# Kernel optimization log

Hardware: AMD Instinct MI355X
Metric: run time of the kernel (lower is better)

Reference implementation:

```python
import jax, jax.numpy as jnp
import numpy as np
import math

ROPE_BASE = 10000.0
ALIBI_SLOPE = 2.0 ** (-8.0)  # _get_alibi_slopes(1) == [2**(-8*1/1)]


def _rope_cos_sin(T, d):
    inv_freq = 1.0 / (ROPE_BASE ** (jnp.arange(0, d, 2, dtype=jnp.float32) / d))
    t = jnp.arange(T, dtype=jnp.float32)
    freqs = jnp.einsum('i,j->ij', t, inv_freq)          # [T, d/2]
    emb = jnp.concatenate([freqs, freqs], axis=-1)      # [T, d]
    return jnp.cos(emb), jnp.sin(emb)


def _rotate_half(x):
    x1, x2 = jnp.split(x, 2, axis=-1)
    return jnp.concatenate([-x2, x1], axis=-1)


def setup_inputs() -> dict:
    key = jax.random.key(0)
    kq, kk, kv = jax.random.split(key, 3)
    B, T, H = 8, 2048, 256
    return {
        'q': jax.random.normal(kq, (B, T, H), dtype=jnp.float32),
        'k': jax.random.normal(kk, (B, T, H), dtype=jnp.float32),
        'v': jax.random.normal(kv, (B, T, H), dtype=jnp.float32),
    }


def reference(q, k, v):
    B, T, H = q.shape  # num_heads == 1, so head_dim == H
    cos, sin = _rope_cos_sin(T, H)                      # [T, H]
    qe = q * cos + _rotate_half(q) * sin                # [B, T, H]
    ke = k * cos + _rotate_half(k) * sin                # [B, T, H]

    scale = 1.0 / math.sqrt(H)
    scores = jnp.einsum('btd,bsd->bts', qe, ke) * scale  # [B, T, T]

    pos = jnp.arange(T)
    rel = (pos[None, :] - pos[:, None]).astype(jnp.float32)  # [T, T]
    alibi = (ALIBI_SLOPE * rel)[None, None, :, :]            # [1, 1, T, T]

    # torch broadcast: [B,T,T] + [1,1,T,T] -> [1,B,T,T]
    scores = scores + alibi
    attn = jax.nn.softmax(scores, axis=-1)              # [1, B, T, T]
    out = jnp.matmul(attn, v)                           # [1, B, T, H]
    return out
```

## Files before the change

kernel.cpp:

```cpp
#include <hip/hip_runtime.h>

#define B_ 8
#define T_ 2048
#define H_ 256
#define PSTR 40
#define SCALE2 0.0901684403f
#define SLOPE2 0.00563552752f
#define ELEMS ((size_t)B_ * T_ * H_)

typedef __attribute__((ext_vector_type(8))) short bf16x8;
typedef __attribute__((ext_vector_type(4))) float f32x4;

#define MFMA16(a, b, c) __builtin_amdgcn_mfma_f32_16x16x32_bf16((a), (b), (c), 0, 0, 0)

__device__ __forceinline__ ushort f2bf(float f) {
  unsigned u = __float_as_uint(f);
  u += 0x7FFFu + ((u >> 16) & 1u);
  return (ushort)(u >> 16);
}

__device__ __forceinline__ void gl_lds16(const ushort* g, ushort* l) {
  __builtin_amdgcn_global_load_lds(
      (const __attribute__((address_space(1))) unsigned int*)g,
      (__attribute__((address_space(3))) unsigned int*)l, 16, 0, 0);
}

__global__ void prep_kernel(const float* __restrict__ k, const float* __restrict__ v,
                            ushort* __restrict__ kt, ushort* __restrict__ vt) {
  __shared__ ushort tile[64][72];
  const int bid = blockIdx.x;
  const int tid = threadIdx.x;
  if (bid < 1024) {
    int idx = bid * 256 + tid;
    int d8 = idx & 15;
    int bt = idx >> 4;
    int t = bt & (T_ - 1);
    int b = bt >> 11;
    size_t base = (size_t)bt * H_ + d8 * 8;
    float4 a0 = *(const float4*)(k + base);
    float4 a1 = *(const float4*)(k + base + 4);
    float4 c0 = *(const float4*)(k + base + 128);
    float4 c1 = *(const float4*)(k + base + 132);
    float av[8] = {a0.x, a0.y, a0.z, a0.w, a1.x, a1.y, a1.z, a1.w};
    float cv[8] = {c0.x, c0.y, c0.z, c0.w, c1.x, c1.y, c1.z, c1.w};
    bf16x8 lo, hi;
#pragma unroll
    for (int e = 0; e < 8; ++e) {
      int j = d8 * 8 + e;
      float rv = (float)t * exp2f((float)j * -0.103810252959f) * 0.15915494309f;
      float fr = rv - floorf(rv);
      float sn = __builtin_amdgcn_sinf(fr), cs = __builtin_amdgcn_cosf(fr);
      lo[e] = (short)f2bf(av[e] * cs - cv[e] * sn);
      hi[e] = (short)f2bf(cv[e] * cs + av[e] * sn);
    }
    size_t kdst = (((size_t)(b * 64 + (t >> 5)) * 32 + d8) * 32 + (t & 31)) * 8;
    *(bf16x8*)(kt + kdst) = lo;
    *(bf16x8*)(kt + kdst + 4096) = hi;
  } else {
    int bid2 = bid - 1024;
    int b = bid2 >> 7, rem = bid2 & 127;
    int h0 = (rem >> 5) * 64, t0 = (rem & 31) * 64;
    int c4 = tid & 15, r0 = tid >> 4;
#pragma unroll
    for (int p = 0; p < 4; ++p) {
      int row = r0 + p * 16;
      const float4 f = *(const float4*)(v + ((size_t)(b * T_ + t0 + row)) * H_ + h0 + c4 * 4);
      ushort4 u;
      u.x = f2bf(f.x); u.y = f2bf(f.y); u.z = f2bf(f.z); u.w = f2bf(f.w);
      *(ushort4*)&tile[row][(c4 * 4) ^ (8 * ((row >> 3) & 7))] = u;
    }
    __syncthreads();
#pragma unroll
    for (int p = 0; p < 2; ++p) {
      int c = tid + p * 256;
      int h = c >> 3, tc = (c & 7) * 8;
      int xo = 8 * (c & 7);
      ushort4 u0, u1;
      u0.x = tile[tc + 0][h ^ xo]; u0.y = tile[tc + 1][h ^ xo];
      u0.z = tile[tc + 2][h ^ xo]; u0.w = tile[tc + 3][h ^ xo];
      u1.x = tile[tc + 4][h ^ xo]; u1.y = tile[tc + 5][h ^ xo];
      u1.z = tile[tc + 6][h ^ xo]; u1.w = tile[tc + 7][h ^ xo];
      int tg = t0 + tc;
      size_t dst = (((size_t)(b * 64 + (tg >> 5)) * 4 + ((tg >> 3) & 3)) * 256 + (h0 + h)) * 8;
      *(ushort4*)(vt + dst) = u0;
      *(ushort4*)(vt + dst + 4) = u1;
    }
  }
}

__global__ __launch_bounds__(512, 4)
void attn_kernel(const float* __restrict__ q, const ushort* __restrict__ kt,
                 const ushort* __restrict__ vt, float* __restrict__ out,
                 float* __restrict__ opart, float* __restrict__ lpart) {
  __shared__ ushort Ksh[2][8192];
  __shared__ ushort Vsh[2][8192];
  __shared__ ushort Psh[8][16 * PSTR];

  const int tid = threadIdx.x;
  const int w = tid >> 6, lane = tid & 63, quad = lane >> 4, l16 = lane & 15;
  const int b = blockIdx.x;
  const int q0 = blockIdx.y * 128;
  const int sp = blockIdx.z;
  const int S = gridDim.z;
  const int niter = (T_ / 32) / S;
  const int kvb = sp * (T_ / S);

  bf16x8 aq[8];
  {
    const float* qb = q + ((size_t)(b * T_) + q0 + w * 16) * H_;
    const int t = q0 + w * 16 + l16;
    float qv[8][8];
#pragma unroll
    for (int ks = 0; ks < 8; ++ks) {
      float4 x0 = *(const float4*)(qb + (size_t)l16 * H_ + ks * 32 + quad * 8);
      float4 x1 = *(const float4*)(qb + (size_t)l16 * H_ + ks * 32 + quad * 8 + 4);
      qv[ks][0] = x0.x; qv[ks][1] = x0.y; qv[ks][2] = x0.z; qv[ks][3] = x0.w;
      qv[ks][4] = x1.x; qv[ks][5] = x1.y; qv[ks][6] = x1.z; qv[ks][7] = x1.w;
    }
#pragma unroll
    for (int ks = 0; ks < 4; ++ks)
#pragma unroll
      for (int e = 0; e < 8; ++e) {
        int d = ks * 32 + quad * 8 + e;
        float rv = (float)t * exp2f((float)d * -0.103810252959f) * 0.15915494309f;
        float fr = rv - floorf(rv);
        float sn = __builtin_amdgcn_sinf(fr), cs = __builtin_amdgcn_cosf(fr);
        aq[ks][e]     = (short)f2bf(qv[ks][e] * cs - qv[ks + 4][e] * sn);
        aq[ks + 4][e] = (short)f2bf(qv[ks + 4][e] * cs + qv[ks][e] * sn);
      }
  }

  const f32x4 fzero = {0.f, 0.f, 0.f, 0.f};
  f32x4 O[16], lac = fzero;
#pragma unroll
  for (int ht = 0; ht < 16; ++ht) O[ht] = fzero;
  bf16x8 vones;
#pragma unroll
  for (int i = 0; i < 8; ++i) vones[i] = (short)0x3F80;

  const ushort* ktb = kt + (size_t)(b * 64 + sp * niter) * 8192;
  const ushort* vtb = vt + (size_t)(b * 64 + sp * niter) * 8192;
  const int stoff = tid * 8;

#pragma unroll
  for (int tt = 0; tt < 2; ++tt) {
    const ushort* kg = ktb + (size_t)tt * 8192;
    const ushort* vg = vtb + (size_t)tt * 8192;
    gl_lds16(kg + stoff, &Ksh[tt][stoff]);
    gl_lds16(kg + stoff + 4096, &Ksh[tt][stoff + 4096]);
    gl_lds16(vg + stoff, &Vsh[tt][stoff]);
    gl_lds16(vg + stoff + 4096, &Vsh[tt][stoff + 4096]);
  }

  const float arb = SLOPE2 * (float)(q0 + w * 16 + quad * 4);

  for (int it = 0; it < niter; ++it) {
    const int p = it & 1;
    __builtin_amdgcn_sched_barrier(0);
    if (it == niter - 1) __builtin_amdgcn_s_waitcnt(0x0070);
    else                 __builtin_amdgcn_s_waitcnt(0x0F74);
    __builtin_amdgcn_s_barrier();
    __builtin_amdgcn_sched_barrier(0);

    f32x4 s[2] = {fzero, fzero};
#pragma unroll
    for (int ks = 0; ks < 8; ++ks)
#pragma unroll
      for (int nt = 0; nt < 2; ++nt) {
        bf16x8 kf = *(const bf16x8*)&Ksh[p][((ks * 4 + quad) * 32 + nt * 16 + l16) * 8];
        s[nt] = MFMA16(aq[ks], kf, s[nt]);
      }

#pragma unroll
    for (int nt = 0; nt < 2; ++nt) {
      float ac = SLOPE2 * (float)(kvb + it * 32 + nt * 16 + l16);
#pragma unroll
      for (int r = 0; r < 4; ++r) {
        float a0 = ac - arb - SLOPE2 * (float)r;
        float pv = __builtin_amdgcn_exp2f(fmaf(s[nt][r], SCALE2, a0));
        Psh[w][(quad * 4 + r) * PSTR + nt * 16 + l16] = f2bf(pv);
      }
    }

    bf16x8 pf = *(const bf16x8*)&Psh[w][l16 * PSTR + quad * 8];
    lac = MFMA16(pf, vones, lac);
#pragma unroll
    for (int ht = 0; ht < 16; ++ht) {
      bf16x8 vf = *(const bf16x8*)&Vsh[p][(quad * 256 + ht * 16 + l16) * 8];
      O[ht] = MFMA16(pf, vf, O[ht]);
    }

    __builtin_amdgcn_sched_barrier(0);
    __builtin_amdgcn_s_waitcnt(0xC07F);
    __builtin_amdgcn_s_barrier();
    __builtin_amdgcn_sched_barrier(0);

    if (it < niter - 2) {
      const ushort* kg = ktb + (size_t)(it + 2) * 8192;
      const ushort* vg = vtb + (size_t)(it + 2) * 8192;
      gl_lds16(kg + stoff, &Ksh[p][stoff]);
      gl_lds16(kg + stoff + 4096, &Ksh[p][stoff + 4096]);
      gl_lds16(vg + stoff, &Vsh[p][stoff]);
      gl_lds16(vg + stoff + 4096, &Vsh[p][stoff + 4096]);
    }
  }

  float* od = (sp == 0) ? out : (opart + (size_t)(sp - 1) * ELEMS);
  float* ob = od + ((size_t)(b * T_) + q0 + w * 16) * H_;
#pragma unroll
  for (int r = 0; r < 4; ++r) {
    int row = quad * 4 + r;
#pragma unroll
    for (int ht = 0; ht < 16; ++ht)
      ob[(size_t)row * H_ + ht * 16 + l16] = O[ht][r];
  }
  if (l16 == 0) {
#pragma unroll
    for (int r = 0; r < 4; ++r)
      lpart[(size_t)(sp * B_ + b) * T_ + q0 + w * 16 + quad * 4 + r] = lac[r];
  }
}

__global__ void combine_kernel(float* __restrict__ out, const float* __restrict__ opart,
                               const float* __restrict__ lpart, int S) {
  int idx = blockIdx.x * 256 + threadIdx.x;
  int row = idx >> 6;
  float l = lpart[row];
  for (int s = 1; s < S; ++s) l += lpart[(size_t)s * B_ * T_ + row];
  float inv = 1.0f / l;
  float4 a = ((const float4*)out)[idx];
  for (int s = 1; s < S; ++s) {
    float4 c = ((const float4*)opart)[(size_t)(s - 1) * (ELEMS / 4) + idx];
    a.x += c.x; a.y += c.y; a.z += c.z; a.w += c.w;
  }
  a.x *= inv; a.y *= inv; a.z *= inv; a.w *= inv;
  ((float4*)out)[idx] = a;
}

extern "C" void kernel_launch(void* const* d_in, const int* in_sizes, int n_in,
                              void* d_out, int out_size, void* d_ws, size_t ws_size,
                              hipStream_t stream) {
  const float* q = (const float*)d_in[0];
  const float* k = (const float*)d_in[1];
  const float* v = (const float*)d_in[2];
  float* out = (float*)d_out;

  ushort* kt = (ushort*)d_ws;
  ushort* vt = kt + ELEMS;
  float* opart = (float*)(vt + ELEMS);
  const size_t need4 = ELEMS * 4 + 3 * ELEMS * 4 + (size_t)4 * B_ * T_ * 4;
  const int S = (ws_size >= need4) ? 4 : 2;
  float* lpart = opart + (size_t)(S - 1) * ELEMS;

  prep_kernel<<<dim3(2048), 256, 0, stream>>>(k, v, kt, vt);
  attn_kernel<<<dim3(B_, T_ / 128, S), 512, 0, stream>>>(q, kt, vt, out, opart, lpart);
  combine_kernel<<<dim3((B_ * T_ * H_ / 4) / 256), 256, 0, stream>>>(out, opart, lpart, S);
}
```

Baseline: 153.4 us.

## Halve attention block to 64 queries and drop K/V double buffering

Each attention block now covers 64 query rows with 4 waves instead of 128 rows with 8, which doubles the grid size. K/V tiles are single-buffered in LDS, so the next tile is loaded only after the barrier that ends the current iteration, which roughly halves LDS use per block. The aim is to fit more blocks per CU and get more parallelism. In exchange, load latency is no longer hidden by prefetching inside a block, and total K/V traffic from global memory doubles because twice as many blocks each stream the same K/V.

```diff
diff --git a/kernel.cpp b/kernel.cpp
--- a/kernel.cpp
+++ b/kernel.cpp
@@ -88,18 +88,18 @@
   }
 }
 
-__global__ __launch_bounds__(512, 4)
+__global__ __launch_bounds__(256, 4)
 void attn_kernel(const float* __restrict__ q, const ushort* __restrict__ kt,
                  const ushort* __restrict__ vt, float* __restrict__ out,
                  float* __restrict__ opart, float* __restrict__ lpart) {
-  __shared__ ushort Ksh[2][8192];
-  __shared__ ushort Vsh[2][8192];
-  __shared__ ushort Psh[8][16 * PSTR];
+  __shared__ ushort Ksh[8192];
+  __shared__ ushort Vsh[8192];
+  __shared__ ushort Psh[4][16 * PSTR];
 
   const int tid = threadIdx.x;
   const int w = tid >> 6, lane = tid & 63, quad = lane >> 4, l16 = lane & 15;
   const int b = blockIdx.x;
-  const int q0 = blockIdx.y * 128;
+  const int q0 = blockIdx.y * 64;
   const int sp = blockIdx.z;
   const int S = gridDim.z;
   const int niter = (T_ / 32) / S;
@@ -138,27 +138,21 @@
 #pragma unroll
   for (int i = 0; i < 8; ++i) vones[i] = (short)0x3F80;
 
-  const ushort* ktb = kt + (size_t)(b * 64 + sp * niter) * 8192;
-  const ushort* vtb = vt + (size_t)(b * 64 + sp * niter) * 8192;
+  const ushort* ktb = kt + (size_t)(b * 64 + sp * (64 / S)) * 8192;
+  const ushort* vtb = vt + (size_t)(b * 64 + sp * (64 / S)) * 8192;
   const int stoff = tid * 8;
 
 #pragma unroll
-  for (int tt = 0; tt < 2; ++tt) {
-    const ushort* kg = ktb + (size_t)tt * 8192;
-    const ushort* vg = vtb + (size_t)tt * 8192;
-    gl_lds16(kg + stoff, &Ksh[tt][stoff]);
-    gl_lds16(kg + stoff + 4096, &Ksh[tt][stoff + 4096]);
-    gl_lds16(vg + stoff, &Vsh[tt][stoff]);
-    gl_lds16(vg + stoff + 4096, &Vsh[tt][stoff + 4096]);
+  for (int i = 0; i < 4; ++i) {
+    gl_lds16(ktb + stoff + i * 2048, &Ksh[stoff + i * 2048]);
+    gl_lds16(vtb + stoff + i * 2048, &Vsh[stoff + i * 2048]);
   }
 
   const float arb = SLOPE2 * (float)(q0 + w * 16 + quad * 4);
 
   for (int it = 0; it < niter; ++it) {
-    const int p = it & 1;
-    __builtin_amdgcn_sched_barrier(0);
-    if (it == niter - 1) __builtin_amdgcn_s_waitcnt(0x0070);
-    else                 __builtin_amdgcn_s_waitcnt(0x0F74);
+    __builtin_amdgcn_sched_barrier(0);
+    __builtin_amdgcn_s_waitcnt(0x0F70);
     __builtin_amdgcn_s_barrier();
     __builtin_amdgcn_sched_barrier(0);
 
@@ -167,7 +161,7 @@
     for (int ks = 0; ks < 8; ++ks)
 #pragma unroll
       for (int nt = 0; nt < 2; ++nt) {
-        bf16x8 kf = *(const bf16x8*)&Ksh[p][((ks * 4 + quad) * 32 + nt * 16 + l16) * 8];
+        bf16x8 kf = *(const bf16x8*)&Ksh[((ks * 4 + quad) * 32 + nt * 16 + l16) * 8];
         s[nt] = MFMA16(aq[ks], kf, s[nt]);
       }
 
@@ -186,7 +180,7 @@
     lac = MFMA16(pf, vones, lac);
 #pragma unroll
     for (int ht = 0; ht < 16; ++ht) {
-      bf16x8 vf = *(const bf16x8*)&Vsh[p][(quad * 256 + ht * 16 + l16) * 8];
+      bf16x8 vf = *(const bf16x8*)&Vsh[(quad * 256 + ht * 16 + l16) * 8];
       O[ht] = MFMA16(pf, vf, O[ht]);
     }
 
@@ -195,13 +189,14 @@
     __builtin_amdgcn_s_barrier();
     __builtin_amdgcn_sched_barrier(0);
 
-    if (it < niter - 2) {
-      const ushort* kg = ktb + (size_t)(it + 2) * 8192;
-      const ushort* vg = vtb + (size_t)(it + 2) * 8192;
-      gl_lds16(kg + stoff, &Ksh[p][stoff]);
-      gl_lds16(kg + stoff + 4096, &Ksh[p][stoff + 4096]);
-      gl_lds16(vg + stoff, &Vsh[p][stoff]);
-      gl_lds16(vg + stoff + 4096, &Vsh[p][stoff + 4096]);
+    if (it < niter - 1) {
+      const ushort* kg = ktb + (size_t)(it + 1) * 8192;
+      const ushort* vg = vtb + (size_t)(it + 1) * 8192;
+#pragma unroll
+      for (int i = 0; i < 4; ++i) {
+        gl_lds16(kg + stoff + i * 2048, &Ksh[stoff + i * 2048]);
+        gl_lds16(vg + stoff + i * 2048, &Vsh[stoff + i * 2048]);
+      }
     }
   }
 
@@ -253,6 +248,6 @@
   float* lpart = opart + (size_t)(S - 1) * ELEMS;
 
   prep_kernel<<<dim3(2048), 256, 0, stream>>>(k, v, kt, vt);
-  attn_kernel<<<dim3(B_, T_ / 128, S), 512, 0, stream>>>(q, kt, vt, out, opart, lpart);
+  attn_kernel<<<dim3(B_, T_ / 64, S), 256, 0, stream>>>(q, kt, vt, out, opart, lpart);
   combine_kernel<<<dim3((B_ * T_ * H_ / 4) / 256), 256, 0, stream>>>(out, opart, lpart, S);
 }
```

After: 162.2 us. +5.7%, slower.
